# Kernel tuning notes

Measured on AMD Instinct MI355X. Metric: run time of the kernel, lower is better.

The kernel has to match this reference:

```python
import jax, jax.numpy as jnp
import numpy as np

B, S, D, H = 8, 2048, 64, 4
Dh = D // H  # head_dim = 16


def setup_inputs() -> dict:
    key = jax.random.key(0)
    k1, k2, k3, k4 = jax.random.split(key, 4)
    x = jax.random.normal(k1, (B, S, D), jnp.float32)
    # Linear weights stored torch-style as [out_features, in_features]
    W_qkv = jax.random.normal(k2, (3 * D, D), jnp.float32) * 0.125
    W_proj = jax.random.normal(k3, (D, D), jnp.float32) * 0.125
    b_proj = jnp.zeros((D,), jnp.float32)
    # Ragged structure: random valid length per sample, causal + padding mask
    lens = jax.random.randint(k4, (B,), S // 4, S + 1)
    pos = jnp.arange(S)
    key_valid = pos[None, :] < lens[:, None]          # [B, S]
    causal = pos[:, None] >= pos[None, :]             # [S, S]
    attn_mask = (causal[None, :, :] & key_valid[:, None, :])[:, None, :, :]  # [B,1,S,S], True=attend
    return {"x": x, "attn_mask": attn_mask, "W_qkv": W_qkv, "W_proj": W_proj, "b_proj": b_proj}


def reference(x, attn_mask, W_qkv, W_proj, b_proj):
    b, s, d = x.shape
    # fused QKV projection (qkv_bias=False)
    qkv = x @ W_qkv.T                                  # [B, S, 3D]
    qkv = qkv.reshape(b, s, 3, H, Dh).transpose(2, 0, 3, 1, 4)  # [3, B, H, S, Dh]
    q, k, v = qkv[0], qkv[1], qkv[2]
    scale = 1.0 / jnp.sqrt(jnp.asarray(Dh, x.dtype))
    scores = jnp.einsum('bhqd,bhkd->bhqk', q, k) * scale  # [B, H, S, S]
    neg = jnp.asarray(jnp.finfo(scores.dtype).min, scores.dtype)
    scores = jnp.where(attn_mask, scores, neg)
    attn = jax.nn.softmax(scores, axis=-1)
    ctx = jnp.einsum('bhqk,bhkd->bhqd', attn, v)       # [B, H, S, Dh]
    ctx = ctx.transpose(0, 2, 1, 3).reshape(b, s, d)   # [B, S, D]
    return ctx @ W_proj.T + b_proj
```

## Files before the change

kernel.cpp:

```cpp
#include <hip/hip_runtime.h>
#include <hip/hip_bf16.h>

typedef __attribute__((ext_vector_type(4))) float f32x4;
typedef __attribute__((ext_vector_type(16))) float f32x16;
typedef __attribute__((ext_vector_type(8))) short bf16x8;
typedef __attribute__((ext_vector_type(4))) short bf16x4;
typedef __attribute__((ext_vector_type(4))) unsigned u32x4;

#define SEQ 2048
#define NH 4
#define DH 16

#define WS_LEN 0
#define WS_WP  1024
#define WS_Q   65536
#define WS_K   (WS_Q + 2097152)
#define WS_V   (WS_K + 2097152)

#define MFMA16 __builtin_amdgcn_mfma_f32_16x16x32_bf16
#define MFMA32 __builtin_amdgcn_mfma_f32_32x32x16_bf16

__device__ __forceinline__ short f2bf(float f){
  __hip_bfloat16 h = __float2bfloat16(f);
  return __builtin_bit_cast(short, h);
}

__device__ __forceinline__ bf16x8 pack8(f32x4 a, f32x4 b){
  bf16x8 r;
  r[0]=f2bf(a[0]); r[1]=f2bf(a[1]); r[2]=f2bf(a[2]); r[3]=f2bf(a[3]);
  r[4]=f2bf(b[0]); r[5]=f2bf(b[1]); r[6]=f2bf(b[2]); r[7]=f2bf(b[3]);
  return r;
}

__device__ __forceinline__ unsigned cvtpk(float a, float b){
  unsigned r;
  asm("v_cvt_pk_bf16_f32 %0, %1, %2" : "=v"(r) : "v"(a), "v"(b));
  return r;
}
__device__ __forceinline__ void plswap(unsigned &a, unsigned &b){
  asm volatile("v_permlane32_swap_b32 %0, %1" : "+v"(a), "+v"(b));
}

__global__ __launch_bounds__(256) void qkv_prep_kernel(const float* __restrict__ x,
                                                       const unsigned char* __restrict__ mask,
                                                       const float* __restrict__ wqkv,
                                                       const float* __restrict__ wproj,
                                                       unsigned char* __restrict__ ws){
  const int tid = threadIdx.x;
  if (blockIdx.x == 256){
    if (blockIdx.y == 1){
      short* wp = (short*)(ws + WS_WP);
      for (int i = tid; i < 64*64; i += 256) wp[i] = f2bf(wproj[i]);
      return;
    }
    const unsigned w0 = *(const unsigned*)mask;
    const int mode = (mask[2048] != 0) ? 0 : ((w0 == 1u) ? 1 : ((w0 == 0x3f800000u) ? 2 : 0));
    __shared__ int cnts[8];
    if (tid < 8) cnts[tid] = 0;
    __syncthreads();
    const int b = tid >> 5, j = tid & 31;
    const long long rowbase = (long long)b * SEQ * SEQ + (long long)(SEQ-1) * SEQ;
    int c = 0;
    if (mode == 0){
      const unsigned* mw = (const unsigned*)(mask + rowbase);
      for (int k = j; k < SEQ/4; k += 32){
        unsigned v = mw[k];
        c += (v & 0xffu ? 1:0) + (v & 0xff00u ? 1:0) + (v & 0xff0000u ? 1:0) + (v & 0xff000000u ? 1:0);
      }
    } else if (mode == 1){
      for (int k = j; k < SEQ; k += 32) c += ((const int*)mask)[rowbase + k] != 0;
    } else {
      for (int k = j; k < SEQ; k += 32) c += ((const float*)mask)[rowbase + k] != 0.0f;
    }
    atomicAdd(&cnts[b], c);
    __syncthreads();
    if (tid < 8) ((int*)ws)[tid] = cnts[tid];
    return;
  }

  const int lane = tid & 63;
  const int wv   = tid >> 6;
  const int c    = lane & 15;
  const int g    = lane >> 4;
  const int T0   = blockIdx.x * 64 + wv * 16;
  const f32x4 z = {0.f, 0.f, 0.f, 0.f};

  bf16x8 aw[2];
  {
    const float* xr = x + (long long)(T0 + c) * 64 + g * 8;
    #pragma unroll
    for (int w = 0; w < 2; ++w){
      f32x4 lo = *(const f32x4*)(xr + w*32);
      f32x4 hi = *(const f32x4*)(xr + w*32 + 4);
      aw[w] = pack8(lo, hi);
    }
  }

  const int tokbase = T0 + g*4;
  const int b = tokbase >> 11;
  const int sbase = tokbase & (SEQ-1);
  short* Qd = (short*)(ws + WS_Q);
  short* Kd = (short*)(ws + WS_K);
  short* Vd = (short*)(ws + WS_V);

  #pragma unroll
  for (int oi = 0; oi < 6; ++oi){
    const int ot = blockIdx.y * 6 + oi;
    const float* wr = wqkv + (ot*16 + c) * 64 + g * 8;
    bf16x8 b0 = pack8(*(const f32x4*)(wr),      *(const f32x4*)(wr + 4));
    bf16x8 b1 = pack8(*(const f32x4*)(wr + 32), *(const f32x4*)(wr + 36));
    f32x4 acc = z;
    acc = MFMA16(aw[0], b0, acc, 0, 0, 0);
    acc = MFMA16(aw[1], b1, acc, 0, 0, 0);
    if (ot < 4){
      short* dst = Qd + ((long long)(b*NH + ot) * SEQ) * DH + c;
      #pragma unroll
      for (int r = 0; r < 4; ++r)
        dst[(long long)(sbase + r) * DH] = f2bf(acc[r] * (0.25f * 1.44269504f));
    } else if (ot < 8){
      short* dst = Kd + ((long long)(b*NH + (ot-4)) * SEQ) * DH + c;
      #pragma unroll
      for (int r = 0; r < 4; ++r)
        dst[(long long)(sbase + r) * DH] = f2bf(acc[r]);
    } else {
      bf16x4 pk;
      #pragma unroll
      for (int r = 0; r < 4; ++r) pk[r] = f2bf(acc[r]);
      *(bf16x4*)(Vd + ((long long)(b*NH + (ot-8)) * DH + c) * SEQ + sbase) = pk;
    }
  }
}

__global__ __launch_bounds__(512, 4) void attn_kernel(const unsigned char* __restrict__ ws,
                                                      const float* __restrict__ bproj,
                                                      float* __restrict__ out){
  const int tid  = threadIdx.x;
  const int lane = tid & 63;
  const int wv   = tid >> 6;
  const int h    = wv & 3;
  const int half = wv >> 2;
  const int c    = lane & 15;
  const int g    = lane >> 4;
  const int ql   = lane & 31;
  const int hi   = lane >> 5;
  const int L    = blockIdx.x;
  const int b    = (L + (L >> 8)) & 7;
  const int u    = L >> 3;
  const int t    = (u < 32) ? (2*u) : (63 - 2*(u - 32));
  const int q0   = t * 32;
  const int len  = ((const int*)ws)[b];
  const long long bh = (long long)(b*NH + h);
  const short* Q  = (const short*)(ws + WS_Q) + bh * SEQ * DH;
  const short* K  = (const short*)(ws + WS_K) + bh * SEQ * DH;
  const short* Vt = (const short*)(ws + WS_V) + bh * DH * SEQ;
  const short* Wp = (const short*)(ws + WS_WP);

  __shared__ __align__(16) unsigned char smem[13328];
  float* CMB = (float*)(smem);
  float* LSB = (float*)(smem + 8704);
  const unsigned CTXB = 9216;
  const f32x4 z  = {0.f,0.f,0.f,0.f};
  const f32x16 z16 = {0.f,0.f,0.f,0.f,0.f,0.f,0.f,0.f,0.f,0.f,0.f,0.f,0.f,0.f,0.f,0.f};
  const short one_bf = (short)0x3F80;
  const bf16x8 zs = {0,0,0,0,0,0,0,0};
  const bf16x8 ones = {one_bf,one_bf,one_bf,one_bf,one_bf,one_bf,one_bf,one_bf};

  const bf16x8 qf = *(const bf16x8*)(Q + (q0 + ql)*DH + hi*8);
  const bf16x8 constv = (ql == 16) ? ones : zs;
  const bool  nlt16 = ql < 16;
  const short* vrow = Vt + (ql & 15)*SEQ;

  f32x16 accD = z16;
  const int kcount = min(q0 + 32, len);
  const int nkt  = (kcount + 63) >> 6;
  const int icnt = min(q0 >> 6, len >> 6);
  const int nh0  = nkt >> 1;
  const int kb   = half ? nh0 : 0;
  const int ke   = half ? nkt : nh0;
  const int qg   = q0 + ql;
  const unsigned sw = (unsigned)(c & 7) << 4;

  bf16x8 ka[2];
  if (kb < ke){
    const int k0 = kb * 64;
    ka[0] = *(const bf16x8*)(K + (k0 + ql)*DH + hi*8);
    ka[1] = *(const bf16x8*)(K + (k0 + 32 + ql)*DH + hi*8);
  }

  for (int kt = kb; kt < ke; ++kt){
    const int k0 = kt * 64;
    bf16x8 vld[4];
    #pragma unroll
    for (int cc = 0; cc < 4; ++cc)
      vld[cc] = *(const bf16x8*)(vrow + k0 + cc*16 + hi*8);
    bf16x8 kan[2];
    if (kt + 1 < ke){
      const int k1 = k0 + 64;
      kan[0] = *(const bf16x8*)(K + (k1 + ql)*DH + hi*8);
      kan[1] = *(const bf16x8*)(K + (k1 + 32 + ql)*DH + hi*8);
    }
    const bool nomask = kt < icnt;

    const f32x16 st0 = MFMA32(ka[0], qf, z16, 0, 0, 0);
    const f32x16 st1 = MFMA32(ka[1], qf, z16, 0, 0, 0);

    #pragma unroll
    for (int kb32 = 0; kb32 < 2; ++kb32){
      const f32x16 st = kb32 ? st1 : st0;
      float p[16];
      #pragma unroll
      for (int j = 0; j < 16; ++j){
        float e = __builtin_amdgcn_exp2f(st[j]);
        if (!nomask){
          const int k = k0 + kb32*32 + (j&3) + 8*(j>>2) + 4*hi;
          e = (k <= qg && k < len) ? e : 0.f;
        }
        p[j] = e;
      }
      unsigned W[8];
      #pragma unroll
      for (int i = 0; i < 8; ++i) W[i] = cvtpk(p[2*i], p[2*i+1]);
      unsigned x0=W[0], y0=W[2]; plswap(x0, y0);
      unsigned x1=W[1], y1=W[3]; plswap(x1, y1);
      unsigned x2=W[4], y2=W[6]; plswap(x2, y2);
      unsigned x3=W[5], y3=W[7]; plswap(x3, y3);
      u32x4 uA = {x0, x1, y0, y1};
      u32x4 uB = {x2, x3, y2, y3};
      const bf16x8 fragA = __builtin_bit_cast(bf16x8, uA);
      const bf16x8 fragB = __builtin_bit_cast(bf16x8, uB);
      const bf16x8 vf0 = nlt16 ? vld[kb32*2 + 0] : constv;
      const bf16x8 vf1 = nlt16 ? vld[kb32*2 + 1] : constv;
      accD = MFMA32(fragA, vf0, accD, 0, 0, 0);
      accD = MFMA32(fragB, vf1, accD, 0, 0, 0);
    }
    ka[0] = kan[0]; ka[1] = kan[1];
  }

  if (half == 0){
    #pragma unroll
    for (int r = 0; r < 16; ++r){
      const int q = (r&3) + 8*(r>>2) + 4*hi;
      if (nlt16)        CMB[(h*32 + q)*17 + ql] = accD[r];
      else if (ql == 16) LSB[h*32 + q] = accD[r];
    }
  }
  __syncthreads();
  if (half == 1){
    #pragma unroll
    for (int r = 0; r < 16; ++r){
      const int q = (r&3) + 8*(r>>2) + 4*hi;
      const float osum = __shfl(accD[r], (lane & 32) | 16);
      if (nlt16){
        const float tot = accD[r] + CMB[(h*32 + q)*17 + ql];
        const float lsT = LSB[h*32 + q] + osum;
        const float cv  = tot / lsT;
        *(short*)&smem[CTXB + q*128 +
            (((unsigned)((h*16 + ql)*2)) ^ ((unsigned)(q & 7) << 4))] = f2bf(cv);
      }
    }
  }
  __syncthreads();

  bf16x8 wpf[2];
  #pragma unroll
  for (int w = 0; w < 2; ++w)
    wpf[w] = *(const bf16x8*)(Wp + (h*16 + c)*64 + w*32 + g*8);
  const float bias = bproj[h*16 + c];
  f32x4 oa = z;
  const unsigned rbc = CTXB + (half*16 + c)*128;
  #pragma unroll
  for (int w = 0; w < 2; ++w){
    bf16x8 pa = *(const bf16x8*)&smem[rbc + ((unsigned)(w*64 + g*16) ^ sw)];
    oa = MFMA16(pa, wpf[w], oa, 0, 0, 0);
  }
  #pragma unroll
  for (int r = 0; r < 4; ++r)
    out[((long long)b * SEQ + q0 + half*16 + g*4 + r) * 64 + h*16 + c] = oa[r] + bias;
}

extern "C" void kernel_launch(void* const* d_in, const int* in_sizes, int n_in,
                              void* d_out, int out_size, void* d_ws, size_t ws_size,
                              hipStream_t stream) {
  const float* x     = (const float*)d_in[0];
  const unsigned char* mask = (const unsigned char*)d_in[1];
  const float* wqkv  = (const float*)d_in[2];
  const float* wproj = (const float*)d_in[3];
  const float* bproj = (const float*)d_in[4];
  float* out = (float*)d_out;
  unsigned char* ws = (unsigned char*)d_ws;

  qkv_prep_kernel<<<dim3(257, 2), 256, 0, stream>>>(x, mask, wqkv, wproj, ws);
  attn_kernel<<<512, 512, 0, stream>>>(ws, bproj, out);
}
```

Baseline: 38.62 us.

## Software-pipeline attention loop, load ones/zeros V rows from workspace, transpose QKV stores

Restructures the attention inner loop into a software pipeline. The softmax probabilities for tile kt+1 are computed while the PV MFMAs for tile kt run, K is prefetched two tiles ahead and V one tile ahead, and the PV MFMAs are wrapped in s_setprio. The per-lane select between V data and a ones/zeros constant is replaced by pointing lanes 16-31 at a ones/zeros row written to the workspace by the prep kernel. The QKV projection swaps its MFMA operands so Q and K are written as packed 4-element vectors, while V is now written with scalar stores. The pipeline raises register pressure, and the extra prefetches add load traffic.

```diff
diff --git a/kernel.cpp b/kernel.cpp
--- a/kernel.cpp
+++ b/kernel.cpp
@@ -11,11 +11,12 @@
 #define NH 4
 #define DH 16
 
-#define WS_LEN 0
-#define WS_WP  1024
-#define WS_Q   65536
-#define WS_K   (WS_Q + 2097152)
-#define WS_V   (WS_K + 2097152)
+#define WS_LEN   0
+#define WS_WP    1024
+#define WS_CONST 16384
+#define WS_Q     65536
+#define WS_K     (WS_Q + 2097152)
+#define WS_V     (WS_K + 2097152)
 
 #define MFMA16 __builtin_amdgcn_mfma_f32_16x16x32_bf16
 #define MFMA32 __builtin_amdgcn_mfma_f32_32x32x16_bf16
@@ -51,6 +52,8 @@
     if (blockIdx.y == 1){
       short* wp = (short*)(ws + WS_WP);
       for (int i = tid; i < 64*64; i += 256) wp[i] = f2bf(wproj[i]);
+      short* cst = (short*)(ws + WS_CONST);
+      for (int i = tid; i < 2048; i += 256){ cst[i] = (short)0x3F80; cst[2048 + i] = 0; }
       return;
     }
     const unsigned w0 = *(const unsigned*)mask;
@@ -96,9 +99,9 @@
     }
   }
 
-  const int tokbase = T0 + g*4;
-  const int b = tokbase >> 11;
-  const int sbase = tokbase & (SEQ-1);
+  const int tok  = T0 + c;
+  const int b    = tok >> 11;
+  const int s    = tok & (SEQ-1);
   short* Qd = (short*)(ws + WS_Q);
   short* Kd = (short*)(ws + WS_K);
   short* Vd = (short*)(ws + WS_V);
@@ -110,23 +113,22 @@
     bf16x8 b0 = pack8(*(const f32x4*)(wr),      *(const f32x4*)(wr + 4));
     bf16x8 b1 = pack8(*(const f32x4*)(wr + 32), *(const f32x4*)(wr + 36));
     f32x4 acc = z;
-    acc = MFMA16(aw[0], b0, acc, 0, 0, 0);
-    acc = MFMA16(aw[1], b1, acc, 0, 0, 0);
+    acc = MFMA16(b0, aw[0], acc, 0, 0, 0);
+    acc = MFMA16(b1, aw[1], acc, 0, 0, 0);
     if (ot < 4){
-      short* dst = Qd + ((long long)(b*NH + ot) * SEQ) * DH + c;
+      bf16x4 pk;
+      #pragma unroll
+      for (int r = 0; r < 4; ++r) pk[r] = f2bf(acc[r] * (0.25f * 1.44269504f));
+      *(bf16x4*)(Qd + ((long long)(b*NH + ot) * SEQ + s) * DH + g*4) = pk;
+    } else if (ot < 8){
+      bf16x4 pk;
+      #pragma unroll
+      for (int r = 0; r < 4; ++r) pk[r] = f2bf(acc[r]);
+      *(bf16x4*)(Kd + ((long long)(b*NH + (ot-4)) * SEQ + s) * DH + g*4) = pk;
+    } else {
       #pragma unroll
       for (int r = 0; r < 4; ++r)
-        dst[(long long)(sbase + r) * DH] = f2bf(acc[r] * (0.25f * 1.44269504f));
-    } else if (ot < 8){
-      short* dst = Kd + ((long long)(b*NH + (ot-4)) * SEQ) * DH + c;
-      #pragma unroll
-      for (int r = 0; r < 4; ++r)
-        dst[(long long)(sbase + r) * DH] = f2bf(acc[r]);
-    } else {
-      bf16x4 pk;
-      #pragma unroll
-      for (int r = 0; r < 4; ++r) pk[r] = f2bf(acc[r]);
-      *(bf16x4*)(Vd + ((long long)(b*NH + (ot-8)) * DH + c) * SEQ + sbase) = pk;
+        Vd[((long long)(b*NH + (ot-8)) * DH + g*4 + r) * SEQ + s] = f2bf(acc[r]);
     }
   }
 }
@@ -154,6 +156,7 @@
   const short* K  = (const short*)(ws + WS_K) + bh * SEQ * DH;
   const short* Vt = (const short*)(ws + WS_V) + bh * DH * SEQ;
   const short* Wp = (const short*)(ws + WS_WP);
+  const short* Cst = (const short*)(ws + WS_CONST);
 
   __shared__ __align__(16) unsigned char smem[13328];
   float* CMB = (float*)(smem);
@@ -161,14 +164,10 @@
   const unsigned CTXB = 9216;
   const f32x4 z  = {0.f,0.f,0.f,0.f};
   const f32x16 z16 = {0.f,0.f,0.f,0.f,0.f,0.f,0.f,0.f,0.f,0.f,0.f,0.f,0.f,0.f,0.f,0.f};
-  const short one_bf = (short)0x3F80;
-  const bf16x8 zs = {0,0,0,0,0,0,0,0};
-  const bf16x8 ones = {one_bf,one_bf,one_bf,one_bf,one_bf,one_bf,one_bf,one_bf};
 
   const bf16x8 qf = *(const bf16x8*)(Q + (q0 + ql)*DH + hi*8);
-  const bf16x8 constv = (ql == 16) ? ones : zs;
   const bool  nlt16 = ql < 16;
-  const short* vrow = Vt + (ql & 15)*SEQ;
+  const short* vrow = nlt16 ? (Vt + ql*SEQ) : (ql == 16 ? Cst : Cst + 2048);
 
   f32x16 accD = z16;
   const int kcount = min(q0 + 32, len);
@@ -180,33 +179,13 @@
   const int qg   = q0 + ql;
   const unsigned sw = (unsigned)(c & 7) << 4;
 
-  bf16x8 ka[2];
-  if (kb < ke){
-    const int k0 = kb * 64;
-    ka[0] = *(const bf16x8*)(K + (k0 + ql)*DH + hi*8);
-    ka[1] = *(const bf16x8*)(K + (k0 + 32 + ql)*DH + hi*8);
-  }
-
-  for (int kt = kb; kt < ke; ++kt){
-    const int k0 = kt * 64;
-    bf16x8 vld[4];
-    #pragma unroll
-    for (int cc = 0; cc < 4; ++cc)
-      vld[cc] = *(const bf16x8*)(vrow + k0 + cc*16 + hi*8);
-    bf16x8 kan[2];
-    if (kt + 1 < ke){
-      const int k1 = k0 + 64;
-      kan[0] = *(const bf16x8*)(K + (k1 + ql)*DH + hi*8);
-      kan[1] = *(const bf16x8*)(K + (k1 + 32 + ql)*DH + hi*8);
-    }
-    const bool nomask = kt < icnt;
-
-    const f32x16 st0 = MFMA32(ka[0], qf, z16, 0, 0, 0);
-    const f32x16 st1 = MFMA32(ka[1], qf, z16, 0, 0, 0);
-
+  auto produce = [&](int tt, bf16x8 k0f, bf16x8 k1f,
+                     bf16x8 (&fA)[2], bf16x8 (&fB)[2]){
+    const int k0 = tt * 64;
+    const bool nomask = tt < icnt;
     #pragma unroll
     for (int kb32 = 0; kb32 < 2; ++kb32){
-      const f32x16 st = kb32 ? st1 : st0;
+      f32x16 st = MFMA32(kb32 ? k1f : k0f, qf, z16, 0, 0, 0);
       float p[16];
       #pragma unroll
       for (int j = 0; j < 16; ++j){
@@ -226,21 +205,60 @@
       unsigned x3=W[5], y3=W[7]; plswap(x3, y3);
       u32x4 uA = {x0, x1, y0, y1};
       u32x4 uB = {x2, x3, y2, y3};
-      const bf16x8 fragA = __builtin_bit_cast(bf16x8, uA);
-      const bf16x8 fragB = __builtin_bit_cast(bf16x8, uB);
-      const bf16x8 vf0 = nlt16 ? vld[kb32*2 + 0] : constv;
-      const bf16x8 vf1 = nlt16 ? vld[kb32*2 + 1] : constv;
-      accD = MFMA32(fragA, vf0, accD, 0, 0, 0);
-      accD = MFMA32(fragB, vf1, accD, 0, 0, 0);
-    }
-    ka[0] = kan[0]; ka[1] = kan[1];
+      fA[kb32] = __builtin_bit_cast(bf16x8, uA);
+      fB[kb32] = __builtin_bit_cast(bf16x8, uB);
+    }
+  };
+
+  bf16x8 ka0, ka1, kan0, kan1, vld[4], vldn[4];
+  bf16x8 fragA[2], fragB[2];
+  if (kb < ke){
+    const int k0 = kb * 64;
+    ka0 = *(const bf16x8*)(K + (k0 + ql)*DH + hi*8);
+    ka1 = *(const bf16x8*)(K + (k0 + 32 + ql)*DH + hi*8);
+    #pragma unroll
+    for (int cc = 0; cc < 4; ++cc)
+      vld[cc] = *(const bf16x8*)(vrow + k0 + cc*16 + hi*8);
+    produce(kb, ka0, ka1, fragA, fragB);
+    if (kb + 1 < ke){
+      const int k1 = k0 + 64;
+      ka0 = *(const bf16x8*)(K + (k1 + ql)*DH + hi*8);
+      ka1 = *(const bf16x8*)(K + (k1 + 32 + ql)*DH + hi*8);
+    }
+  }
+
+  for (int kt = kb; kt < ke; ++kt){
+    if (kt + 2 < ke){
+      const int k2 = (kt + 2) * 64;
+      kan0 = *(const bf16x8*)(K + (k2 + ql)*DH + hi*8);
+      kan1 = *(const bf16x8*)(K + (k2 + 32 + ql)*DH + hi*8);
+    }
+    if (kt + 1 < ke){
+      const int k1 = (kt + 1) * 64;
+      #pragma unroll
+      for (int cc = 0; cc < 4; ++cc)
+        vldn[cc] = *(const bf16x8*)(vrow + k1 + cc*16 + hi*8);
+    }
+
+    __builtin_amdgcn_s_setprio(1);
+    accD = MFMA32(fragA[0], vld[0], accD, 0, 0, 0);
+    accD = MFMA32(fragB[0], vld[1], accD, 0, 0, 0);
+    accD = MFMA32(fragA[1], vld[2], accD, 0, 0, 0);
+    accD = MFMA32(fragB[1], vld[3], accD, 0, 0, 0);
+    __builtin_amdgcn_s_setprio(0);
+
+    if (kt + 1 < ke) produce(kt + 1, ka0, ka1, fragA, fragB);
+
+    ka0 = kan0; ka1 = kan1;
+    #pragma unroll
+    for (int cc = 0; cc < 4; ++cc) vld[cc] = vldn[cc];
   }
 
   if (half == 0){
     #pragma unroll
     for (int r = 0; r < 16; ++r){
       const int q = (r&3) + 8*(r>>2) + 4*hi;
-      if (nlt16)        CMB[(h*32 + q)*17 + ql] = accD[r];
+      if (nlt16)         CMB[(h*32 + q)*17 + ql] = accD[r];
       else if (ql == 16) LSB[h*32 + q] = accD[r];
     }
   }
```

Measured after the change: 38.95 us. Within noise of the previous version (+0.9%).
